# Performance work log

Hardware: AMD Instinct MI355X
Metric: run time of the kernel (lower is better)

Reference implementation:

```python
import jax, jax.numpy as jnp
import numpy as np

NUM_ROWS = 16384
H = 2048
K = 4
EXPERT_NUM = 64


def setup_inputs() -> dict:
    key = jax.random.key(0)
    k1, k2, k3 = jax.random.split(key, 3)
    x = jax.random.normal(k1, (NUM_ROWS, H), dtype=jnp.float32)
    expert_idx = jax.random.randint(k2, (NUM_ROWS, K), 0, EXPERT_NUM, dtype=jnp.int32)
    scale = jax.random.uniform(k3, (NUM_ROWS,), dtype=jnp.float32)
    return {"x": x, "expert_idx": expert_idx, "scale": scale, "expert_num": EXPERT_NUM}


def reference(x, expert_idx, scale, expert_num):
    # Dropless MoE token routing (drop_pad_mode=0, active_num=0 -> all tokens,
    # quant_mode=-1 with scale, expert_tokens_num_type=1, full active range).
    num_rows, h = x.shape
    k = expert_idx.shape[-1]
    n = num_rows * k
    eidx = expert_idx.reshape(-1)                     # [n]
    sorted_idx = jnp.argsort(eidx, stable=True)       # stable sort by expert id
    src_row = sorted_idx // k                         # original token row per expanded slot
    expanded_x = x[src_row]                           # [n, h] gathered tokens, expert-grouped
    # inverse permutation: position of each original (row,k) slot in the expanded output
    expanded_row_idx = jnp.zeros((n,), dtype=jnp.int32).at[sorted_idx].set(
        jnp.arange(n, dtype=jnp.int32))
    expert_tokens_count = jnp.bincount(eidx, length=expert_num).astype(jnp.int32)
    expanded_scale = scale[src_row].astype(jnp.float32)  # [n]
    return expanded_x, expanded_row_idx, expert_tokens_count, expanded_scale
```

## Files before the change

### kernel.cpp

```cpp
#include <hip/hip_runtime.h>

#define NROWS   16384
#define HDIM    2048
#define TOPK    4
#define NEXP    64
#define NSLOT   (NROWS * TOPK)
#define SLOTS_PER_BLOCK 256
#define NBLK    (NSLOT / SLOTS_PER_BLOCK)

__global__ void hist_kernel(const int* __restrict__ eidx, int* __restrict__ hist) {
    __shared__ int h[NEXP];
    int t = threadIdx.x;
    if (t < NEXP) h[t] = 0;
    __syncthreads();
    int slot = blockIdx.x * SLOTS_PER_BLOCK + t;
    int e = eidx[slot];
    atomicAdd(&h[e], 1);
    __syncthreads();
    if (t < NEXP) hist[blockIdx.x * NEXP + t] = h[t];
}

__global__ void scan_kernel(const int* __restrict__ hist, int* __restrict__ base,
                            float* __restrict__ out_counts) {
    int e = threadIdx.x;
    int total = 0;
    #pragma unroll 8
    for (int b = 0; b < NBLK; ++b) total += hist[b * NEXP + e];
    out_counts[e] = (float)total;

    int incl = total;
    #pragma unroll
    for (int d = 1; d < 64; d <<= 1) {
        int y = __shfl_up(incl, d, 64);
        if (e >= d) incl += y;
    }
    int running = incl - total;
    for (int b = 0; b < NBLK; ++b) {
        base[b * NEXP + e] = running;
        running += hist[b * NEXP + e];
    }
}

__global__ void rank_kernel(const int* __restrict__ eidx, const int* __restrict__ base,
                            const float* __restrict__ scale,
                            int* __restrict__ dest_ws, float* __restrict__ out_idx,
                            float* __restrict__ out_scale) {
    __shared__ int se[SLOTS_PER_BLOCK];
    int t = threadIdx.x;
    int slot = blockIdx.x * SLOTS_PER_BLOCK + t;
    int e = eidx[slot];
    se[t] = e;
    __syncthreads();
    int rank = 0;
    #pragma unroll 8
    for (int i = 0; i < SLOTS_PER_BLOCK; ++i) {
        int v = se[i];
        rank += (i < t && v == e) ? 1 : 0;
    }
    int dest = base[blockIdx.x * NEXP + e] + rank;
    dest_ws[slot] = dest;
    out_idx[slot] = (float)dest;
    out_scale[dest] = scale[slot >> 2];
}

__global__ void __launch_bounds__(256) copy_kernel(const float4* __restrict__ x,
                                                   const int* __restrict__ dest_ws,
                                                   float4* __restrict__ out) {
    int slot = blockIdx.x;
    int dest = dest_ws[slot];
    int src  = slot >> 2;
    const float4* xs = x   + (size_t)src  * (HDIM / 4);
    float4*       od = out + (size_t)dest * (HDIM / 4);
    int t = threadIdx.x;
    od[t]       = xs[t];
    od[t + 256] = xs[t + 256];
}

extern "C" void kernel_launch(void* const* d_in, const int* in_sizes, int n_in,
                              void* d_out, int out_size, void* d_ws, size_t ws_size,
                              hipStream_t stream) {
    const float* x     = (const float*)d_in[0];
    const int*   eidx  = (const int*)d_in[1];
    const float* scale = (const float*)d_in[2];

    float* out        = (float*)d_out;
    float* out_x      = out;
    float* out_idx    = out + (size_t)NSLOT * HDIM;
    float* out_counts = out_idx + NSLOT;
    float* out_scale  = out_counts + NEXP;

    int* hist = (int*)d_ws;
    int* base = hist + NBLK * NEXP;
    int* dest = base + NBLK * NEXP;

    hist_kernel<<<NBLK, SLOTS_PER_BLOCK, 0, stream>>>(eidx, hist);
    scan_kernel<<<1, 64, 0, stream>>>(hist, base, out_counts);
    rank_kernel<<<NBLK, SLOTS_PER_BLOCK, 0, stream>>>(eidx, base, scale,
                                                      dest, out_idx, out_scale);
    copy_kernel<<<NSLOT, 256, 0, stream>>>((const float4*)x, dest, (float4*)out_x);
}
```

Measured before the change: 664.2 us.

## Parallelize expert scan and copy each source row once to all four destinations

New measurement: 637.5 us. -4.0%, faster.

```diff
diff --git a/kernel.cpp b/kernel.cpp
--- a/kernel.cpp
+++ b/kernel.cpp
@@ -7,6 +7,10 @@
 #define NSLOT   (NROWS * TOPK)
 #define SLOTS_PER_BLOCK 256
 #define NBLK    (NSLOT / SLOTS_PER_BLOCK)
+#define CHUNK   16
+#define NCHUNK  (NBLK / CHUNK)
+
+typedef float f4 __attribute__((ext_vector_type(4)));
 
 __global__ void hist_kernel(const int* __restrict__ eidx, int* __restrict__ hist) {
     __shared__ int h[NEXP];
@@ -20,24 +24,50 @@
     if (t < NEXP) hist[blockIdx.x * NEXP + t] = h[t];
 }
 
-__global__ void scan_kernel(const int* __restrict__ hist, int* __restrict__ base,
-                            float* __restrict__ out_counts) {
-    int e = threadIdx.x;
-    int total = 0;
-    #pragma unroll 8
-    for (int b = 0; b < NBLK; ++b) total += hist[b * NEXP + e];
-    out_counts[e] = (float)total;
+__global__ void __launch_bounds__(1024) scan_kernel(const int* __restrict__ hist,
+                                                    int* __restrict__ base,
+                                                    float* __restrict__ out_counts) {
+    __shared__ int partial[NCHUNK][NEXP];
+    __shared__ int expert_off[NEXP];
+    int tid = threadIdx.x;
+    int c = tid >> 6;
+    int e = tid & 63;
+    int b0 = c * CHUNK;
 
-    int incl = total;
+    int s = 0;
     #pragma unroll
-    for (int d = 1; d < 64; d <<= 1) {
-        int y = __shfl_up(incl, d, 64);
-        if (e >= d) incl += y;
+    for (int i = 0; i < CHUNK; ++i) s += hist[(b0 + i) * NEXP + e];
+    partial[c][e] = s;
+    __syncthreads();
+
+    int excl = 0;
+    #pragma unroll
+    for (int i = 0; i < NCHUNK; ++i) {
+        int v = partial[i][e];
+        excl += (i < c) ? v : 0;
     }
-    int running = incl - total;
-    for (int b = 0; b < NBLK; ++b) {
-        base[b * NEXP + e] = running;
-        running += hist[b * NEXP + e];
+
+    if (tid < 64) {
+        int total = 0;
+        #pragma unroll
+        for (int i = 0; i < NCHUNK; ++i) total += partial[i][tid];
+        out_counts[tid] = (float)total;
+        int incl = total;
+        #pragma unroll
+        for (int d = 1; d < 64; d <<= 1) {
+            int y = __shfl_up(incl, d, 64);
+            if (tid >= d) incl += y;
+        }
+        expert_off[tid] = incl - total;
+    }
+    __syncthreads();
+
+    int running = expert_off[e] + excl;
+    #pragma unroll
+    for (int i = 0; i < CHUNK; ++i) {
+        int idx = (b0 + i) * NEXP + e;
+        base[idx] = running;
+        running += hist[idx];
     }
 }
 
@@ -63,17 +93,27 @@
     out_scale[dest] = scale[slot >> 2];
 }
 
-__global__ void __launch_bounds__(256) copy_kernel(const float4* __restrict__ x,
+__global__ void __launch_bounds__(256) copy_kernel(const f4* __restrict__ x,
                                                    const int* __restrict__ dest_ws,
-                                                   float4* __restrict__ out) {
-    int slot = blockIdx.x;
-    int dest = dest_ws[slot];
-    int src  = slot >> 2;
-    const float4* xs = x   + (size_t)src  * (HDIM / 4);
-    float4*       od = out + (size_t)dest * (HDIM / 4);
+                                                   f4* __restrict__ out) {
+    int row = blockIdx.x;
     int t = threadIdx.x;
-    od[t]       = xs[t];
-    od[t + 256] = xs[t + 256];
+    const f4* xs = x + (size_t)row * (HDIM / 4);
+    f4 v0 = __builtin_nontemporal_load(xs + t);
+    f4 v1 = __builtin_nontemporal_load(xs + t + 256);
+    const int4 d = *reinterpret_cast<const int4*>(dest_ws + ((size_t)row << 2));
+    f4* o0 = out + (size_t)d.x * (HDIM / 4);
+    f4* o1 = out + (size_t)d.y * (HDIM / 4);
+    f4* o2 = out + (size_t)d.z * (HDIM / 4);
+    f4* o3 = out + (size_t)d.w * (HDIM / 4);
+    __builtin_nontemporal_store(v0, o0 + t);
+    __builtin_nontemporal_store(v1, o0 + t + 256);
+    __builtin_nontemporal_store(v0, o1 + t);
+    __builtin_nontemporal_store(v1, o1 + t + 256);
+    __builtin_nontemporal_store(v0, o2 + t);
+    __builtin_nontemporal_store(v1, o2 + t + 256);
+    __builtin_nontemporal_store(v0, o3 + t);
+    __builtin_nontemporal_store(v1, o3 + t + 256);
 }
 
 extern "C" void kernel_launch(void* const* d_in, const int* in_sizes, int n_in,
@@ -94,8 +134,8 @@
     int* dest = base + NBLK * NEXP;
 
     hist_kernel<<<NBLK, SLOTS_PER_BLOCK, 0, stream>>>(eidx, hist);
-    scan_kernel<<<1, 64, 0, stream>>>(hist, base, out_counts);
+    scan_kernel<<<1, 1024, 0, stream>>>(hist, base, out_counts);
     rank_kernel<<<NBLK, SLOTS_PER_BLOCK, 0, stream>>>(eidx, base, scale,
                                                       dest, out_idx, out_scale);
-    copy_kernel<<<NSLOT, 256, 0, stream>>>((const float4*)x, dest, (float4*)out_x);
+    copy_kernel<<<NROWS, 256, 0, stream>>>((const f4*)x, dest, (f4*)out_x);
 }
```
